# Optimization experiments

Measured on AMD Instinct MI355X. Metric: run time of the kernel, lower is better.

The kernel has to match this reference:

```python
import jax, jax.numpy as jnp
import numpy as np

B, T, D = 1, 2048, 1024
H = 16
SEM_DIM, GEO_DIM, ATTN_DIM = 512, 512, 1024
ROPE_BASE = 10000.0
NEG = -1e9


def setup_inputs() -> dict:
    key = jax.random.key(0)
    ks = jax.random.split(key, 10)
    s = 0.02
    return {
        "x": jax.random.normal(ks[0], (B, T, D), jnp.float32),
        "wq_sem": jax.random.normal(ks[1], (D, SEM_DIM), jnp.float32) * s,
        "wk_sem": jax.random.normal(ks[2], (D, SEM_DIM), jnp.float32) * s,
        "wq_geo": jax.random.normal(ks[3], (D, GEO_DIM), jnp.float32) * s,
        "wk_geo": jax.random.normal(ks[4], (D, GEO_DIM), jnp.float32) * s,
        "wv": jax.random.normal(ks[5], (D, ATTN_DIM), jnp.float32) * s,
        "wo": jax.random.normal(ks[6], (ATTN_DIM, D), jnp.float32) * s,
        "k_sem_null": jax.random.normal(ks[7], (SEM_DIM,), jnp.float32) * s,
        "k_geo_null": jax.random.normal(ks[8], (GEO_DIM,), jnp.float32) * s,
        "v_null": jax.random.normal(ks[9], (ATTN_DIM,), jnp.float32) * s,
    }


def _heads(y, hd):
    b, t, _ = y.shape
    return y.reshape(b, t, H, hd).transpose(0, 2, 1, 3)  # [B,H,T,hd]


def _rope(x, cos, sin):
    # x: [B,H,T,hd], cos/sin: [T,hd//2] (rotate-half convention)
    hd = x.shape[-1]
    x1, x2 = x[..., : hd // 2], x[..., hd // 2 :]
    c = cos[None, None]
    sn = sin[None, None]
    return jnp.concatenate([x1 * c - x2 * sn, x2 * c + x1 * sn], axis=-1)


def _forward(x, wq_sem, wk_sem, wq_geo, wk_geo, wv, wo, k_sem_null, k_geo_null, v_null):
    b, t, _ = x.shape
    sem_hd = wq_sem.shape[1] // H
    geo_hd = wq_geo.shape[1] // H
    v_hd = wv.shape[1] // H
    sem_scale = 1.0 / np.sqrt(sem_hd)
    geo_scale = 1.0 / np.sqrt(geo_hd)

    qs = _heads(x @ wq_sem, sem_hd)
    ks = _heads(x @ wk_sem, sem_hd)
    qg = _heads(x @ wq_geo, geo_hd)
    kg = _heads(x @ wk_geo, geo_hd)
    v = _heads(x @ wv, v_hd)

    # RoPE on geometric branch only
    pos = jnp.arange(t, dtype=jnp.float32)
    inv_freq = 1.0 / (ROPE_BASE ** (jnp.arange(0, geo_hd, 2, dtype=jnp.float32) / geo_hd))
    ang = pos[:, None] * inv_freq[None, :]  # [T, geo_hd//2]
    cos, sin = jnp.cos(ang), jnp.sin(ang)
    qg = _rope(qg, cos, sin)
    kg = _rope(kg, cos, sin)

    # prepend null KV slot (not rotated, always attendable)
    ksn = jnp.broadcast_to(k_sem_null.reshape(1, 1, H, sem_hd).transpose(0, 2, 1, 3), (b, H, 1, sem_hd))
    kgn = jnp.broadcast_to(k_geo_null.reshape(1, 1, H, geo_hd).transpose(0, 2, 1, 3), (b, H, 1, geo_hd))
    vn = jnp.broadcast_to(v_null.reshape(1, 1, H, v_hd).transpose(0, 2, 1, 3), (b, H, 1, v_hd))
    ks_full = jnp.concatenate([ksn, ks], axis=2)  # [B,H,T+1,sem_hd]
    kg_full = jnp.concatenate([kgn, kg], axis=2)
    v_full = jnp.concatenate([vn, v], axis=2)

    # decoupled scores in fp32: sem*sem_scale + geo*geo_scale
    scores = (
        jnp.einsum("bhqd,bhkd->bhqk", qs, ks_full).astype(jnp.float32) * sem_scale
        + jnp.einsum("bhqd,bhkd->bhqk", qg, kg_full).astype(jnp.float32) * geo_scale
    )

    # causal mask over real tokens; null slot (key index 0) always visible
    causal = jnp.tril(jnp.ones((t, t), dtype=bool))
    mask = jnp.concatenate([jnp.ones((t, 1), dtype=bool), causal], axis=1)  # [T, T+1]
    scores = jnp.where(mask[None, None], scores, NEG)

    probs = jax.nn.softmax(scores, axis=-1).astype(v.dtype)
    out = jnp.einsum("bhqk,bhkd->bhqd", probs, v_full)  # [B,H,T,v_hd]
    out = out.transpose(0, 2, 1, 3).reshape(b, t, H * v_hd)
    return out @ wo


def reference(x, wq_sem, wk_sem, wq_geo, wk_geo, wv, wo, k_sem_null, k_geo_null, v_null):
    return _forward(x, wq_sem, wk_sem, wq_geo, wk_geo, wv, wo, k_sem_null, k_geo_null, v_null)
```

## Files before the change

kernel.cpp:

```cpp
#include <hip/hip_runtime.h>
#include <hip/hip_bf16.h>

typedef __hip_bfloat16 bf16;
typedef __attribute__((ext_vector_type(8))) short bf16x8;
typedef __attribute__((ext_vector_type(4))) short bf16x4;
typedef __attribute__((ext_vector_type(4))) float f32x4;

#define TSEQ   2048
#define DMODEL 1024
#define NHEAD  16
#define KST    2112
#define SCALE  0.17677669529663687f
#define LN1E4_16 0.5756462732485115f

__device__ __forceinline__ unsigned short f2bf(float f) {
    union { bf16 h; unsigned short u; } x;
    x.h = __float2bfloat16(f);
    return x.u;
}
__device__ __forceinline__ float bf2f(unsigned short u) {
    return __uint_as_float(((unsigned int)u) << 16);
}

__device__ __forceinline__ void gload_lds16(const void* g, void* l) {
    __builtin_amdgcn_global_load_lds(
        (const __attribute__((address_space(1))) void*)g,
        (__attribute__((address_space(3))) void*)l, 16, 0, 0);
}

__global__ __launch_bounds__(256) void prep_all(
    const float* __restrict__ X,
    const float* __restrict__ wqs, const float* __restrict__ wks,
    const float* __restrict__ wqg, const float* __restrict__ wkg,
    const float* __restrict__ wv,  const float* __restrict__ wo,
    const float* __restrict__ ksn, const float* __restrict__ kgn,
    const float* __restrict__ vn,
    unsigned short* __restrict__ Xb,
    unsigned short* __restrict__ WcatT, unsigned short* __restrict__ WoT,
    unsigned short* __restrict__ Kc, unsigned short* __restrict__ Vg)
{
    __shared__ float T[64][65];
    const int bx = blockIdx.x;
    const int tid = threadIdx.x;
    if (bx < 2048) {
        int i = (bx * 256 + tid) * 4;
        float4 v = *(const float4*)(X + i);
        ushort4 o;
        o.x = f2bf(v.x); o.y = f2bf(v.y); o.z = f2bf(v.z); o.w = f2bf(v.w);
        *(ushort4*)(Xb + i) = o;
    } else if (bx < 3584) {
        const int idx = bx - 2048;
        const int z = idx >> 8, rem = idx & 255;
        const int cx = rem & 15, ry = rem >> 4;
        const float* src; unsigned short* dst; int C;
        switch (z) {
            case 0: src = wqs; dst = WcatT;               C = 512;  break;
            case 1: src = wks; dst = WcatT + 512  * 1024; C = 512;  break;
            case 2: src = wqg; dst = WcatT + 1024 * 1024; C = 512;  break;
            case 3: src = wkg; dst = WcatT + 1536 * 1024; C = 512;  break;
            case 4: src = wv;  dst = WcatT + 2048 * 1024; C = 1024; break;
            default: src = wo; dst = WoT;                 C = 1024; break;
        }
        const int c0 = cx * 64;
        if (c0 >= C) return;
        const int r0 = ry * 64;
        #pragma unroll
        for (int i = 0; i < 16; ++i) {
            int id2 = tid + 256 * i;
            int r = id2 >> 6, c = id2 & 63;
            T[r][c] = src[(size_t)(r0 + r) * C + c0 + c];
        }
        __syncthreads();
        #pragma unroll
        for (int i = 0; i < 16; ++i) {
            int id2 = tid + 256 * i;
            int cc = id2 >> 6, rr = id2 & 63;
            dst[(size_t)(c0 + cc) * 1024 + r0 + rr] = f2bf(T[rr][cc]);
        }
    } else {
        const int h = bx - 3584;
        const int d = tid & 63, g = tid >> 6;
        if (g == 0)
            Kc[((size_t)h * KST + 0) * 64 + d] =
                f2bf(d < 32 ? ksn[h * 32 + d] : kgn[h * 32 + d - 32]);
        if (g == 1)
            Vg[((size_t)h * 64 + d) * KST + 0] = f2bf(vn[h * 64 + d]);
        for (int fk = 2049 + g; fk < KST; fk += 4) {
            Kc[((size_t)h * KST + fk) * 64 + d] = 0;
            Vg[((size_t)h * 64 + d) * KST + fk] = 0;
        }
    }
}

__global__ __launch_bounds__(256) void gemm_proj_fused(
    const unsigned short* __restrict__ A,
    const unsigned short* __restrict__ Bt,
    unsigned short* __restrict__ Qc,
    unsigned short* __restrict__ Kc,
    unsigned short* __restrict__ Vg)
{
    __shared__ __align__(16) unsigned short Abuf[64 * 64];
    __shared__ __align__(16) unsigned short Bbuf[128 * 64];
    const int n0 = blockIdx.x * 128, m0 = blockIdx.y * 64;
    const int tid = threadIdx.x, l = tid & 63, wv = tid >> 6;
    const int wr = wv >> 1, wc = wv & 1;
    const int lr = l & 15, lg = l >> 4;

    f32x4 acc[2][4];
    #pragma unroll
    for (int i = 0; i < 2; ++i)
        #pragma unroll
        for (int j = 0; j < 4; ++j) acc[i][j] = (f32x4){0.f, 0.f, 0.f, 0.f};

    for (int k0 = 0; k0 < 1024; k0 += 64) {
        #pragma unroll
        for (int i = 0; i < 2; ++i) {
            int c = wv * 128 + i * 64 + l;
            int row = c >> 3, sseg = (c & 7) ^ (row & 7);
            gload_lds16(A + (size_t)(m0 + row) * 1024 + k0 + sseg * 8,
                        &Abuf[(wv * 128 + i * 64) * 8]);
        }
        #pragma unroll
        for (int i = 0; i < 4; ++i) {
            int c = wv * 256 + i * 64 + l;
            int row = c >> 3, sseg = (c & 7) ^ (row & 7);
            gload_lds16(Bt + (size_t)(n0 + row) * 1024 + k0 + sseg * 8,
                        &Bbuf[(wv * 256 + i * 64) * 8]);
        }
        __syncthreads();
        #pragma unroll
        for (int ks = 0; ks < 2; ++ks) {
            bf16x8 af[2], bfv[4];
            #pragma unroll
            for (int mf = 0; mf < 2; ++mf) {
                int rr = wr * 32 + mf * 16 + lr;
                int seg = (ks * 4 + lg) ^ (rr & 7);
                af[mf] = *(const bf16x8*)&Abuf[rr * 64 + seg * 8];
            }
            #pragma unroll
            for (int nf = 0; nf < 4; ++nf) {
                int rr = wc * 64 + nf * 16 + lr;
                int seg = (ks * 4 + lg) ^ (rr & 7);
                bfv[nf] = *(const bf16x8*)&Bbuf[rr * 64 + seg * 8];
            }
            #pragma unroll
            for (int mf = 0; mf < 2; ++mf)
                #pragma unroll
                for (int nf = 0; nf < 4; ++nf)
                    acc[mf][nf] = __builtin_amdgcn_mfma_f32_16x16x32_bf16(
                        af[mf], bfv[nf], acc[mf][nf], 0, 0, 0);
        }
        __syncthreads();
    }

    const int sec = n0 >> 9;
    if (sec <= 1) {
        unsigned short* dst = (sec == 0) ? Qc : Kc;
        const int tstr  = (sec == 0) ? TSEQ : KST;
        const int fkoff = (sec == 0) ? 0 : 1;
        const float sc  = (sec == 0) ? SCALE : 1.0f;
        #pragma unroll
        for (int mf = 0; mf < 2; ++mf)
            #pragma unroll
            for (int nf = 0; nf < 4; ++nf) {
                int col = (n0 & 511) + wc * 64 + nf * 16 + lr;
                int h = col >> 5, d = col & 31;
                #pragma unroll
                for (int reg = 0; reg < 4; ++reg) {
                    int q = m0 + wr * 32 + mf * 16 + lg * 4 + reg;
                    dst[((size_t)h * tstr + q + fkoff) * 64 + d] =
                        f2bf(acc[mf][nf][reg] * sc);
                }
            }
    } else if (sec <= 3) {
        unsigned short* dst = (sec == 2) ? Qc : Kc;
        const int tstr  = (sec == 2) ? TSEQ : KST;
        const int fkoff = (sec == 2) ? 0 : 1;
        const float sc  = (sec == 2) ? SCALE : 1.0f;
        const float invf = __expf(-(float)lr * LN1E4_16);
        #pragma unroll
        for (int mf = 0; mf < 2; ++mf)
            #pragma unroll
            for (int reg = 0; reg < 4; ++reg) {
                int q = m0 + wr * 32 + mf * 16 + lg * 4 + reg;
                float s, c;
                __sincosf((float)q * invf, &s, &c);
                #pragma unroll
                for (int nfp = 0; nfp < 2; ++nfp) {
                    int nf0 = nfp * 2;
                    int colbase = (n0 & 511) + wc * 64 + nf0 * 16;
                    int h = colbase >> 5;
                    float x1 = acc[mf][nf0][reg], x2 = acc[mf][nf0 + 1][reg];
                    size_t base = ((size_t)h * tstr + q + fkoff) * 64 + 32;
                    dst[base + lr]      = f2bf((x1 * c - x2 * s) * sc);
                    dst[base + lr + 16] = f2bf((x2 * c + x1 * s) * sc);
                }
            }
    } else {
        #pragma unroll
        for (int nf = 0; nf < 4; ++nf) {
            int colr = (n0 - 2048) + wc * 64 + nf * 16 + lr;
            int h = colr >> 6, dv = colr & 63;
            size_t rowbase = ((size_t)h * 64 + dv) * KST;
            #pragma unroll
            for (int mf = 0; mf < 2; ++mf)
                #pragma unroll
                for (int reg = 0; reg < 4; ++reg) {
                    int q = m0 + wr * 32 + mf * 16 + lg * 4 + reg;
                    Vg[rowbase + q + 1] = f2bf(acc[mf][nf][reg]);
                }
        }
    }
}

__global__ __launch_bounds__(256) void gemm_out(const unsigned short* __restrict__ A,
                                                const unsigned short* __restrict__ Bt,
                                                float* __restrict__ C)
{
    __shared__ __align__(16) unsigned short Abuf[64 * 64];
    __shared__ __align__(16) unsigned short Bbuf[128 * 64];
    const int n0 = blockIdx.x * 128, m0 = blockIdx.y * 64;
    const int tid = threadIdx.x, l = tid & 63, wv = tid >> 6;
    const int wr = wv >> 1, wc = wv & 1;
    const int lr = l & 15, lg = l >> 4;

    f32x4 acc[2][4];
    #pragma unroll
    for (int i = 0; i < 2; ++i)
        #pragma unroll
        for (int j = 0; j < 4; ++j) acc[i][j] = (f32x4){0.f, 0.f, 0.f, 0.f};

    for (int k0 = 0; k0 < 1024; k0 += 64) {
        #pragma unroll
        for (int i = 0; i < 2; ++i) {
            int c = wv * 128 + i * 64 + l;
            int row = c >> 3, sseg = (c & 7) ^ (row & 7);
            gload_lds16(A + (size_t)(m0 + row) * 1024 + k0 + sseg * 8,
                        &Abuf[(wv * 128 + i * 64) * 8]);
        }
        #pragma unroll
        for (int i = 0; i < 4; ++i) {
            int c = wv * 256 + i * 64 + l;
            int row = c >> 3, sseg = (c & 7) ^ (row & 7);
            gload_lds16(Bt + (size_t)(n0 + row) * 1024 + k0 + sseg * 8,
                        &Bbuf[(wv * 256 + i * 64) * 8]);
        }
        __syncthreads();
        #pragma unroll
        for (int ks = 0; ks < 2; ++ks) {
            bf16x8 af[2], bfv[4];
            #pragma unroll
            for (int mf = 0; mf < 2; ++mf) {
                int rr = wr * 32 + mf * 16 + lr;
                int seg = (ks * 4 + lg) ^ (rr & 7);
                af[mf] = *(const bf16x8*)&Abuf[rr * 64 + seg * 8];
            }
            #pragma unroll
            for (int nf = 0; nf < 4; ++nf) {
                int rr = wc * 64 + nf * 16 + lr;
                int seg = (ks * 4 + lg) ^ (rr & 7);
                bfv[nf] = *(const bf16x8*)&Bbuf[rr * 64 + seg * 8];
            }
            #pragma unroll
            for (int mf = 0; mf < 2; ++mf)
                #pragma unroll
                for (int nf = 0; nf < 4; ++nf)
                    acc[mf][nf] = __builtin_amdgcn_mfma_f32_16x16x32_bf16(
                        af[mf], bfv[nf], acc[mf][nf], 0, 0, 0);
        }
        __syncthreads();
    }
    #pragma unroll
    for (int mf = 0; mf < 2; ++mf)
        #pragma unroll
        for (int nf = 0; nf < 4; ++nf)
            #pragma unroll
            for (int reg = 0; reg < 4; ++reg) {
                int row = m0 + wr * 32 + mf * 16 + lg * 4 + reg;
                int col = n0 + wc * 64 + nf * 16 + lr;
                C[(size_t)row * DMODEL + col] = acc[mf][nf][reg];
            }
}

__global__ __launch_bounds__(256, 3) void attn_mfma(
    const unsigned short* __restrict__ Qc,
    const unsigned short* __restrict__ Kc,
    const unsigned short* __restrict__ Vg,
    unsigned short* __restrict__ attnO,
    unsigned short* __restrict__ OpA,
    unsigned short* __restrict__ OpB,
    float2* __restrict__ ml)
{
    __shared__ __align__(16) unsigned short KsL[3][64 * 64];
    __shared__ __align__(16) unsigned short VsL[2][64 * 64];
    __shared__ __align__(16) unsigned short Ps[64 * 64];

    const int ib = blockIdx.x;
    const int hp = ib & 7;
    const int j  = ib >> 3;
    const int h  = hp * 2 + (j & 1);
    const int item = j >> 1;

    int qb, part, np;
    {
        int i = item;
        if (i < 16)      { np = 4; qb = 15 - (i >> 2); part = i & 3; }
        else if (i < 28) { int jj = i - 16; np = 3; qb = 11 - jj / 3; part = jj % 3; }
        else if (i < 38) { int jj = i - 28; np = 2; qb = 7 - (jj >> 1); part = jj & 1; }
        else             { np = 1; qb = 2 - (i - 38); part = 0; }
    }
    const int nt = 2 * qb + 3;
    const int bsz = nt / np, rem = nt % np;
    const int t0 = part * bsz + (part < rem ? part : rem);
    const int t1 = t0 + bsz + (part < rem ? 1 : 0);

    const int q0 = qb * 128;
    const int tid = threadIdx.x, l = tid & 63, w = tid >> 6;
    const int lr = l & 15, lg = l >> 4;

    bf16x8 qa[2][2];
    #pragma unroll
    for (int rg = 0; rg < 2; ++rg) {
        int qr = q0 + w * 32 + rg * 16 + lr;
        qa[rg][0] = *(const bf16x8*)&Qc[((size_t)h * TSEQ + qr) * 64 + lg * 8];
        qa[rg][1] = *(const bf16x8*)&Qc[((size_t)h * TSEQ + qr) * 64 + 32 + lg * 8];
    }

    const int sc8 = (((l & 7) ^ ((l >> 3) & 7))) * 8;
    const int r0s = (w * 2 + 0) * 8 + (l >> 3);
    const int r1s = (w * 2 + 1) * 8 + (l >> 3);
    const unsigned short* Kh = Kc + (((size_t)h * KST) << 6);
    const unsigned short* Vh = Vg + (size_t)h * 64 * KST;

#define STAGE_K(bufi, fk0_) do {                                               \
        gload_lds16(Kh + (((size_t)((fk0_) + r0s)) << 6) + sc8,                \
                    &KsL[bufi][(w * 2 + 0) * 512]);                            \
        gload_lds16(Kh + (((size_t)((fk0_) + r1s)) << 6) + sc8,                \
                    &KsL[bufi][(w * 2 + 1) * 512]);                            \
    } while (0)
#define STAGE_V(bufi, fk0_) do {                                               \
        gload_lds16(Vh + (size_t)r0s * KST + (fk0_) + sc8,                     \
                    &VsL[bufi][(w * 2 + 0) * 512]);                            \
        gload_lds16(Vh + (size_t)r1s * KST + (fk0_) + sc8,                     \
                    &VsL[bufi][(w * 2 + 1) * 512]);                            \
    } while (0)

    f32x4 o[2][4];
    #pragma unroll
    for (int rg = 0; rg < 2; ++rg)
        #pragma unroll
        for (int i = 0; i < 4; ++i) o[rg][i] = (f32x4){0.f, 0.f, 0.f, 0.f};
    float m[2]  = {-1e30f, -1e30f};
    float ll[2] = {0.f, 0.f};

    STAGE_K(t0 % 3, t0 * 64);
    STAGE_V(t0 & 1, t0 * 64);
    STAGE_K((t0 + 1) % 3, (t0 + 1) * 64);
    asm volatile("s_waitcnt vmcnt(2)" ::: "memory");
    __builtin_amdgcn_s_barrier();

    for (int kb = t0; kb < t1; ++kb) {
        const int fk0 = kb * 64;
        const unsigned short* Ksb = &KsL[kb % 3][0];
        const unsigned short* Vsb = &VsL[kb & 1][0];
        const bool moreV = (kb + 1 < t1);
        const bool moreK = (kb + 2 < t1);
        if (moreV) STAGE_V((kb + 1) & 1, fk0 + 64);
        if (moreK) STAGE_K((kb + 2) % 3, fk0 + 128);

        bf16x8 vb[2][4];
        #pragma unroll
        for (int ks = 0; ks < 2; ++ks)
            #pragma unroll
            for (int nf = 0; nf < 4; ++nf) {
                int dv = nf * 16 + lr;
                vb[ks][nf] = *(const bf16x8*)
                    &Vsb[dv * 64 + ((lg * 8 + ks * 32) ^ ((dv & 7) << 3))];
            }

        f32x4 sa[2][4];
        #pragma unroll
        for (int rg = 0; rg < 2; ++rg)
            #pragma unroll
            for (int i = 0; i < 4; ++i) sa[rg][i] = (f32x4){0.f, 0.f, 0.f, 0.f};
        #pragma unroll
        for (int ks = 0; ks < 2; ++ks) {
            int dd = lg * 8 + ks * 32;
            #pragma unroll
            for (int nf = 0; nf < 4; ++nf) {
                int kkc = nf * 16 + lr;
                bf16x8 kbf = *(const bf16x8*)&Ksb[kkc * 64 + (dd ^ ((kkc & 7) << 3))];
                sa[0][nf] = __builtin_amdgcn_mfma_f32_16x16x32_bf16(kbf, qa[0][ks], sa[0][nf], 0, 0, 0);
                sa[1][nf] = __builtin_amdgcn_mfma_f32_16x16x32_bf16(kbf, qa[1][ks], sa[1][nf], 0, 0, 0);
            }
        }

        const bool needmask = (fk0 + 62 > q0 + w * 32);
        const int pr = w * 16 + lr;
        const int psw = (pr & 7) << 3;
        #pragma unroll
        for (int rg = 0; rg < 2; ++rg) {
            const int q = q0 + w * 32 + rg * 16 + lr;
            float mt = -1e30f;
            if (needmask) {
                #pragma unroll
                for (int nf = 0; nf < 4; ++nf)
                    #pragma unroll
                    for (int reg = 0; reg < 4; ++reg) {
                        int fk = fk0 + nf * 16 + lg * 4 + reg;
                        float val = (fk <= q + 1) ? sa[rg][nf][reg] : -1e9f;
                        sa[rg][nf][reg] = val;
                        mt = fmaxf(mt, val);
                    }
            } else {
                #pragma unroll
                for (int nf = 0; nf < 4; ++nf)
                    #pragma unroll
                    for (int reg = 0; reg < 4; ++reg)
                        mt = fmaxf(mt, sa[rg][nf][reg]);
            }
            mt = fmaxf(mt, __shfl_xor(mt, 16, 64));
            mt = fmaxf(mt, __shfl_xor(mt, 32, 64));
            if (__any(mt > m[rg] + 8.0f)) {
                float mn = fmaxf(m[rg], mt);
                float alpha = __expf(m[rg] - mn);
                m[rg] = mn;
                ll[rg] *= alpha;
                #pragma unroll
                for (int nf = 0; nf < 4; ++nf)
                    #pragma unroll
                    for (int reg = 0; reg < 4; ++reg)
                        o[rg][nf][reg] *= alpha;
            }
            float rs = 0.0f;
            #pragma unroll
            for (int nf = 0; nf < 4; ++nf)
                #pragma unroll
                for (int reg = 0; reg < 4; ++reg) {
                    float p = __expf(sa[rg][nf][reg] - m[rg]);
                    sa[rg][nf][reg] = p;
                    rs += p;
                }
            rs += __shfl_xor(rs, 16, 64);
            rs += __shfl_xor(rs, 32, 64);
            ll[rg] += rs;

            #pragma unroll
            for (int nf = 0; nf < 4; ++nf) {
                bf16x4 pk;
                pk[0] = f2bf(sa[rg][nf][0]); pk[1] = f2bf(sa[rg][nf][1]);
                pk[2] = f2bf(sa[rg][nf][2]); pk[3] = f2bf(sa[rg][nf][3]);
                int kk0 = nf * 16 + lg * 4;
                *(bf16x4*)&Ps[pr * 64 + (kk0 ^ psw)] = pk;
            }
            #pragma unroll
            for (int ks = 0; ks < 2; ++ks) {
                int kk0 = lg * 8 + ks * 32;
                bf16x8 pa = *(const bf16x8*)&Ps[pr * 64 + (kk0 ^ psw)];
                #pragma unroll
                for (int nf = 0; nf < 4; ++nf)
                    o[rg][nf] = __builtin_amdgcn_mfma_f32_16x16x32_bf16(
                        vb[ks][nf], pa, o[rg][nf], 0, 0, 0);
            }
        }

        if (moreK) { asm volatile("s_waitcnt vmcnt(2)" ::: "memory"); }
        else       { asm volatile("s_waitcnt vmcnt(0)" ::: "memory"); }
        __builtin_amdgcn_s_barrier();
    }
#undef STAGE_K
#undef STAGE_V

    const int sidx = h * 38 + item;
    unsigned short* Od = (np == 1) ? 0
        : ((sidx < 384) ? OpA + (size_t)sidx * 8192
                        : OpB + (size_t)(sidx - 384) * 8192);
    #pragma unroll
    for (int rg = 0; rg < 2; ++rg) {
        const float inv = 1.0f / ll[rg];
        const int q = q0 + w * 32 + rg * 16 + lr;
        if (np == 1) {
            #pragma unroll
            for (int nf = 0; nf < 4; ++nf) {
                ushort4 ov;
                ov.x = f2bf(o[rg][nf][0] * inv); ov.y = f2bf(o[rg][nf][1] * inv);
                ov.z = f2bf(o[rg][nf][2] * inv); ov.w = f2bf(o[rg][nf][3] * inv);
                *(ushort4*)&attnO[(size_t)q * DMODEL + h * 64 + nf * 16 + lg * 4] = ov;
            }
        } else {
            const int r = w * 32 + rg * 16 + lr;
            #pragma unroll
            for (int nf = 0; nf < 4; ++nf) {
                ushort4 ov;
                ov.x = f2bf(o[rg][nf][0] * inv); ov.y = f2bf(o[rg][nf][1] * inv);
                ov.z = f2bf(o[rg][nf][2] * inv); ov.w = f2bf(o[rg][nf][3] * inv);
                *(ushort4*)&Od[r * 64 + nf * 16 + lg * 4] = ov;
            }
            if (lg == 0)
                ml[sidx * 128 + r] = make_float2(m[rg], ll[rg]);
        }
    }
}

__global__ __launch_bounds__(256) void combine_wave(
    const unsigned short* __restrict__ OpA,
    const unsigned short* __restrict__ OpB,
    const float2* __restrict__ ml,
    unsigned short* __restrict__ attnO)
{
    const int qb = 3 + blockIdx.x;
    const int h  = blockIdx.y;
    int np, i0;
    if (qb >= 12)     { np = 4; i0 = (15 - qb) * 4; }
    else if (qb >= 8) { np = 3; i0 = 16 + (11 - qb) * 3; }
    else              { np = 2; i0 = 28 + (7 - qb) * 2; }
    const int sidx0 = h * 38 + i0;

    const int t = threadIdx.x;
    const int r = t & 127, dv0 = (t >> 7) * 32;

    float wt[4];
    float mm = -1e30f;
    #pragma unroll
    for (int p = 0; p < 4; ++p)
        if (p < np) mm = fmaxf(mm, ml[(sidx0 + p) * 128 + r].x);
    float tot = 0.0f;
    #pragma unroll
    for (int p = 0; p < 4; ++p) {
        wt[p] = 0.0f;
        if (p < np) {
            float2 v = ml[(sidx0 + p) * 128 + r];
            wt[p] = v.y * __expf(v.x - mm);
            tot += wt[p];
        }
    }
    const float inv = 1.0f / tot;

    float accv[32];
    #pragma unroll
    for (int c = 0; c < 32; ++c) accv[c] = 0.0f;
    #pragma unroll
    for (int p = 0; p < 4; ++p) {
        if (p < np) {
            int s = sidx0 + p;
            const unsigned short* Od = (s < 384)
                ? OpA + (size_t)s * 8192
                : OpB + (size_t)(s - 384) * 8192;
            #pragma unroll
            for (int c4 = 0; c4 < 8; ++c4) {
                ushort4 v = *(const ushort4*)&Od[r * 64 + dv0 + c4 * 4];
                accv[c4 * 4 + 0] += wt[p] * bf2f(v.x);
                accv[c4 * 4 + 1] += wt[p] * bf2f(v.y);
                accv[c4 * 4 + 2] += wt[p] * bf2f(v.z);
                accv[c4 * 4 + 3] += wt[p] * bf2f(v.w);
            }
        }
    }
    const int q = qb * 128 + r;
    #pragma unroll
    for (int c4 = 0; c4 < 8; ++c4) {
        ushort4 ov;
        ov.x = f2bf(accv[c4 * 4 + 0] * inv);
        ov.y = f2bf(accv[c4 * 4 + 1] * inv);
        ov.z = f2bf(accv[c4 * 4 + 2] * inv);
        ov.w = f2bf(accv[c4 * 4 + 3] * inv);
        *(ushort4*)&attnO[(size_t)q * DMODEL + h * 64 + dv0 + c4 * 4] = ov;
    }
}

extern "C" void kernel_launch(void* const* d_in, const int* in_sizes, int n_in,
                              void* d_out, int out_size, void* d_ws, size_t ws_size,
                              hipStream_t stream)
{
    const float* x      = (const float*)d_in[0];
    const float* wq_sem = (const float*)d_in[1];
    const float* wk_sem = (const float*)d_in[2];
    const float* wq_geo = (const float*)d_in[3];
    const float* wk_geo = (const float*)d_in[4];
    const float* wv     = (const float*)d_in[5];
    const float* wo     = (const float*)d_in[6];
    const float* ksn    = (const float*)d_in[7];
    const float* kgn    = (const float*)d_in[8];
    const float* vn     = (const float*)d_in[9];
    float* out = (float*)d_out;

    char* ws = (char*)d_ws;
    unsigned short* Xb    = (unsigned short*)(ws);
    unsigned short* attnO = (unsigned short*)(ws);
    unsigned short* WcatT = (unsigned short*)(ws + 4194304);
    unsigned short* OpA   = (unsigned short*)(ws + 4194304);
    unsigned short* WoT   = (unsigned short*)(ws + 10485760);
    unsigned short* Qc    = (unsigned short*)(ws + 12582912);
    unsigned short* Kc    = (unsigned short*)(ws + 16777216);
    unsigned short* Vg    = (unsigned short*)(ws + 21102592);
    unsigned short* OpB   = (unsigned short*)(ws + 25427968);
    float2*         ml    = (float2*)(ws + 29097984);

    prep_all<<<3600, 256, 0, stream>>>(x, wq_sem, wk_sem, wq_geo, wk_geo, wv, wo,
                                       ksn, kgn, vn, Xb, WcatT, WoT, Kc, Vg);

    gemm_proj_fused<<<dim3(24, 32), 256, 0, stream>>>(Xb, WcatT, Qc, Kc, Vg);

    attn_mfma<<<656, 256, 0, stream>>>(Qc, Kc, Vg, attnO, OpA, OpB, ml);
    combine_wave<<<dim3(13, NHEAD), 256, 0, stream>>>(OpA, OpB, ml, attnO);

    gemm_out<<<dim3(8, 32), 256, 0, stream>>>(attnO, WoT, out);
}
```

Before: 84.16 us.

## Fuse split-KV combine into attention kernel via last-block atomic counter

Removes the separate combine_wave launch. Each split partition of the attention kernel now increments a per-(head, query-block) atomic counter, and the last partition to finish merges the partial outputs using the stored max and sum values. This saves one kernel launch and its gap. In exchange it adds threadfences, an atomic and extra block-level syncs. It also keeps the combine registers live in the attention kernel, which could reduce occupancy.

Result: slower. 194.2 us (+130.7%).

```diff
diff --git a/kernel.cpp b/kernel.cpp
--- a/kernel.cpp
+++ b/kernel.cpp
@@ -37,7 +37,8 @@
     const float* __restrict__ vn,
     unsigned short* __restrict__ Xb,
     unsigned short* __restrict__ WcatT, unsigned short* __restrict__ WoT,
-    unsigned short* __restrict__ Kc, unsigned short* __restrict__ Vg)
+    unsigned short* __restrict__ Kc, unsigned short* __restrict__ Vg,
+    int* __restrict__ cnt)
 {
     __shared__ float T[64][65];
     const int bx = blockIdx.x;
@@ -80,6 +81,7 @@
     } else {
         const int h = bx - 3584;
         const int d = tid & 63, g = tid >> 6;
+        if (tid < 13) cnt[h * 13 + tid] = 0;
         if (g == 0)
             Kc[((size_t)h * KST + 0) * 64 + d] =
                 f2bf(d < 32 ? ksn[h * 32 + d] : kgn[h * 32 + d - 32]);
@@ -289,11 +291,13 @@
     unsigned short* __restrict__ attnO,
     unsigned short* __restrict__ OpA,
     unsigned short* __restrict__ OpB,
-    float2* __restrict__ ml)
+    float2* __restrict__ ml,
+    int* __restrict__ cnt)
 {
     __shared__ __align__(16) unsigned short KsL[3][64 * 64];
     __shared__ __align__(16) unsigned short VsL[2][64 * 64];
     __shared__ __align__(16) unsigned short Ps[64 * 64];
+    __shared__ int go;
 
     const int ib = blockIdx.x;
     const int hp = ib & 7;
@@ -500,71 +504,72 @@
                 ml[sidx * 128 + r] = make_float2(m[rg], ll[rg]);
         }
     }
-}
-
-__global__ __launch_bounds__(256) void combine_wave(
-    const unsigned short* __restrict__ OpA,
-    const unsigned short* __restrict__ OpB,
-    const float2* __restrict__ ml,
-    unsigned short* __restrict__ attnO)
-{
-    const int qb = 3 + blockIdx.x;
-    const int h  = blockIdx.y;
-    int np, i0;
-    if (qb >= 12)     { np = 4; i0 = (15 - qb) * 4; }
-    else if (qb >= 8) { np = 3; i0 = 16 + (11 - qb) * 3; }
-    else              { np = 2; i0 = 28 + (7 - qb) * 2; }
-    const int sidx0 = h * 38 + i0;
-
-    const int t = threadIdx.x;
-    const int r = t & 127, dv0 = (t >> 7) * 32;
-
-    float wt[4];
-    float mm = -1e30f;
-    #pragma unroll
-    for (int p = 0; p < 4; ++p)
-        if (p < np) mm = fmaxf(mm, ml[(sidx0 + p) * 128 + r].x);
-    float tot = 0.0f;
-    #pragma unroll
-    for (int p = 0; p < 4; ++p) {
-        wt[p] = 0.0f;
-        if (p < np) {
-            float2 v = ml[(sidx0 + p) * 128 + r];
-            wt[p] = v.y * __expf(v.x - mm);
-            tot += wt[p];
-        }
-    }
-    const float inv = 1.0f / tot;
-
-    float accv[32];
-    #pragma unroll
-    for (int c = 0; c < 32; ++c) accv[c] = 0.0f;
-    #pragma unroll
-    for (int p = 0; p < 4; ++p) {
-        if (p < np) {
-            int s = sidx0 + p;
-            const unsigned short* Od = (s < 384)
-                ? OpA + (size_t)s * 8192
-                : OpB + (size_t)(s - 384) * 8192;
+
+    if (np > 1) {
+        __threadfence();
+        __syncthreads();
+        if (tid == 0) {
+            int prev = atomicAdd(&cnt[h * 13 + (qb - 3)], 1);
+            go = (prev == np - 1) ? 1 : 0;
+        }
+        __syncthreads();
+        if (go) {
+            __threadfence();
+            int i0;
+            if (qb >= 12)     i0 = (15 - qb) * 4;
+            else if (qb >= 8) i0 = 16 + (11 - qb) * 3;
+            else              i0 = 28 + (7 - qb) * 2;
+            const int sidx0 = h * 38 + i0;
+            const int r = tid & 127, dv0 = (tid >> 7) * 32;
+
+            float wt[4];
+            float mm = -1e30f;
+            #pragma unroll
+            for (int p = 0; p < 4; ++p)
+                if (p < np) mm = fmaxf(mm, ml[(sidx0 + p) * 128 + r].x);
+            float tot = 0.0f;
+            #pragma unroll
+            for (int p = 0; p < 4; ++p) {
+                wt[p] = 0.0f;
+                if (p < np) {
+                    float2 v = ml[(sidx0 + p) * 128 + r];
+                    wt[p] = v.y * __expf(v.x - mm);
+                    tot += wt[p];
+                }
+            }
+            const float inv = 1.0f / tot;
+
+            float accv[32];
+            #pragma unroll
+            for (int c = 0; c < 32; ++c) accv[c] = 0.0f;
+            #pragma unroll
+            for (int p = 0; p < 4; ++p) {
+                if (p < np) {
+                    int s = sidx0 + p;
+                    const unsigned short* Op = (s < 384)
+                        ? OpA + (size_t)s * 8192
+                        : OpB + (size_t)(s - 384) * 8192;
+                    #pragma unroll
+                    for (int c4 = 0; c4 < 8; ++c4) {
+                        ushort4 v = *(const ushort4*)&Op[r * 64 + dv0 + c4 * 4];
+                        accv[c4 * 4 + 0] += wt[p] * bf2f(v.x);
+                        accv[c4 * 4 + 1] += wt[p] * bf2f(v.y);
+                        accv[c4 * 4 + 2] += wt[p] * bf2f(v.z);
+                        accv[c4 * 4 + 3] += wt[p] * bf2f(v.w);
+                    }
+                }
+            }
+            const int qq = qb * 128 + r;
             #pragma unroll
             for (int c4 = 0; c4 < 8; ++c4) {
-                ushort4 v = *(const ushort4*)&Od[r * 64 + dv0 + c4 * 4];
-                accv[c4 * 4 + 0] += wt[p] * bf2f(v.x);
-                accv[c4 * 4 + 1] += wt[p] * bf2f(v.y);
-                accv[c4 * 4 + 2] += wt[p] * bf2f(v.z);
-                accv[c4 * 4 + 3] += wt[p] * bf2f(v.w);
-            }
-        }
-    }
-    const int q = qb * 128 + r;
-    #pragma unroll
-    for (int c4 = 0; c4 < 8; ++c4) {
-        ushort4 ov;
-        ov.x = f2bf(accv[c4 * 4 + 0] * inv);
-        ov.y = f2bf(accv[c4 * 4 + 1] * inv);
-        ov.z = f2bf(accv[c4 * 4 + 2] * inv);
-        ov.w = f2bf(accv[c4 * 4 + 3] * inv);
-        *(ushort4*)&attnO[(size_t)q * DMODEL + h * 64 + dv0 + c4 * 4] = ov;
+                ushort4 ov;
+                ov.x = f2bf(accv[c4 * 4 + 0] * inv);
+                ov.y = f2bf(accv[c4 * 4 + 1] * inv);
+                ov.z = f2bf(accv[c4 * 4 + 2] * inv);
+                ov.w = f2bf(accv[c4 * 4 + 3] * inv);
+                *(ushort4*)&attnO[(size_t)qq * DMODEL + h * 64 + dv0 + c4 * 4] = ov;
+            }
+        }
     }
 }
 
@@ -595,14 +600,14 @@
     unsigned short* Vg    = (unsigned short*)(ws + 21102592);
     unsigned short* OpB   = (unsigned short*)(ws + 25427968);
     float2*         ml    = (float2*)(ws + 29097984);
+    int*            cnt   = (int*)(ws + 29720576);
 
     prep_all<<<3600, 256, 0, stream>>>(x, wq_sem, wk_sem, wq_geo, wk_geo, wv, wo,
-                                       ksn, kgn, vn, Xb, WcatT, WoT, Kc, Vg);
+                                       ksn, kgn, vn, Xb, WcatT, WoT, Kc, Vg, cnt);
 
     gemm_proj_fused<<<dim3(24, 32), 256, 0, stream>>>(Xb, WcatT, Qc, Kc, Vg);
 
-    attn_mfma<<<656, 256, 0, stream>>>(Qc, Kc, Vg, attnO, OpA, OpB, ml);
-    combine_wave<<<dim3(13, NHEAD), 256, 0, stream>>>(OpA, OpB, ml, attnO);
+    attn_mfma<<<656, 256, 0, stream>>>(Qc, Kc, Vg, attnO, OpA, OpB, ml, cnt);
 
     gemm_out<<<dim3(8, 32), 256, 0, stream>>>(attnO, WoT, out);
 }
```
